# Kernel tuning notes

Measured on AMD Instinct MI355X. Metric: run time of the kernel, lower is better.

## Reference

```python
import jax, jax.numpy as jnp
import numpy as np

EPS = 1e-10

def setup_inputs() -> dict:
    key = jax.random.key(0)
    k0, k1, k2, k3, k4, k5 = jax.random.split(key, 6)
    B, S, V, C, D = 256, 20, 20000, 20, 64
    support_set_images = jax.random.uniform(k0, (B, S, V), dtype=jnp.float32)
    support_set_y_one_hot = jax.nn.one_hot(jax.random.randint(k1, (B, S), 0, C), C, dtype=jnp.float32)
    target_image = jax.random.uniform(k2, (B, V), dtype=jnp.float32)
    target_y = jax.random.randint(k3, (B,), 0, C)
    W = jax.random.normal(k4, (D, V), dtype=jnp.float32) * (1.0 / np.sqrt(V).astype(np.float32))
    b = jax.random.normal(k5, (D,), dtype=jnp.float32) * 0.01
    return dict(support_set_images=support_set_images,
                support_set_y_one_hot=support_set_y_one_hot,
                target_image=target_image, target_y=target_y, W=W, b=b)


def reference(support_set_images, support_set_y_one_hot, target_image, target_y, W, b):
    # SentenceEncoder (Linear vocab->64), applied to each support item and the target.
    sup = jnp.einsum('bsv,dv->bsd', support_set_images, W) + b        # [B,S,64]
    tgt = target_image @ W.T + b                                      # [B,64]

    # DistanceNetwork: dot(target, support) * rsqrt(clamp(||support||^2, eps))
    # (only the support vector's magnitude is normalized -- faithful to source).
    mag = jax.lax.rsqrt(jnp.clip(jnp.sum(sup * sup, axis=-1), EPS, None))  # [B,S]
    dots = jnp.einsum('bsd,bd->bs', sup, tgt)                              # [B,S]
    similarities = dots * mag                                              # [B,S]

    # AttentionalClassify: softmax over support, weighted combine of labels.
    attn = jax.nn.softmax(similarities, axis=-1)                           # [B,S]
    preds = jnp.einsum('bs,bsc->bc', attn, support_set_y_one_hot)          # [B,C]

    indices = jnp.argmax(preds, axis=1)
    accuracy = jnp.mean((indices == target_y).astype(jnp.float32))
    # F.cross_entropy applies log_softmax to preds (even though preds are already pdfs).
    logp = jax.nn.log_softmax(preds, axis=-1)
    crossentropy_loss = -jnp.mean(jnp.take_along_axis(logp, target_y[:, None], axis=1))
    return accuracy, crossentropy_loss
```

## Files before the change

### kernel.cpp

```cpp
#include <hip/hip_runtime.h>
#include <hip/hip_bf16.h>
#include <math.h>

#define B_  256
#define S_  20
#define V_  20000
#define C_  20
#define D_  64
#define MTOT (B_*S_ + B_)
#define KSPLIT 10
#define NK32 625

typedef __bf16 bf16x8 __attribute__((ext_vector_type(8)));
typedef float  f32x4  __attribute__((ext_vector_type(4)));

__device__ __forceinline__ void split8(const float4 a, const float4 b,
                                       uint4& hi, uint4& lo) {
    const float f[8] = {a.x, a.y, a.z, a.w, b.x, b.y, b.z, b.w};
    unsigned int h[8]; float r[8];
#pragma unroll
    for (int j = 0; j < 8; ++j) {
        const unsigned int u = __float_as_uint(f[j]);
        h[j] = u & 0xFFFF0000u;
        r[j] = f[j] - __uint_as_float(h[j]);
    }
    hi.x = (h[0] >> 16) | h[1];
    hi.y = (h[2] >> 16) | h[3];
    hi.z = (h[4] >> 16) | h[5];
    hi.w = (h[6] >> 16) | h[7];
    lo.x = (__float_as_uint(r[0]) >> 16) | (__float_as_uint(r[1]) & 0xFFFF0000u);
    lo.y = (__float_as_uint(r[2]) >> 16) | (__float_as_uint(r[3]) & 0xFFFF0000u);
    lo.z = (__float_as_uint(r[4]) >> 16) | (__float_as_uint(r[5]) & 0xFFFF0000u);
    lo.w = (__float_as_uint(r[6]) >> 16) | (__float_as_uint(r[7]) & 0xFFFF0000u);
}

__global__ __launch_bounds__(256)
void wconv_kernel(const float* __restrict__ W,
                  uint4* __restrict__ Wfh, uint4* __restrict__ Wfl) {
    const int g    = blockIdx.x * 256 + threadIdx.x;
    const int lane = g & 63;
    const int tt   = (g >> 6) & 3;
    const int c    = g >> 8;
    const int ln = lane & 15, qd = lane >> 4;
    const float* src = W + (size_t)(16 * tt + ln) * V_ + c * 32 + qd * 8;
    const float4 a = *(const float4*)src;
    const float4 b = *(const float4*)(src + 4);
    uint4 h, l; split8(a, b, h, l);
    Wfh[g] = h; Wfl[g] = l;
}

__device__ __forceinline__ void ldx(const float* xrow, int c, float4& r0, float4& r1) {
    const float* p = xrow + (size_t)c * 32;
    r0 = *(const float4*)p;
    r1 = *(const float4*)(p + 4);
}
__device__ __forceinline__ void ldw(const uint4* bh, const uint4* bl, int c,
                                    uint4* wh, uint4* wl) {
    const uint4* ph = bh + (size_t)c * 256;
    const uint4* pl = bl + (size_t)c * 256;
#pragma unroll
    for (int tt = 0; tt < 4; ++tt) { wh[tt] = ph[tt * 64]; wl[tt] = pl[tt * 64]; }
}
__device__ __forceinline__ void step(const float4 x0, const float4 x1,
                                     const uint4* wh, const uint4* wl, f32x4* acc) {
    uint4 hu, lu; split8(x0, x1, hu, lu);
    const bf16x8 ah = *(const bf16x8*)&hu;
    const bf16x8 al = *(const bf16x8*)&lu;
#pragma unroll
    for (int tt = 0; tt < 4; ++tt) {
        const bf16x8 bh = *(const bf16x8*)&wh[tt];
        const bf16x8 bl = *(const bf16x8*)&wl[tt];
        acc[tt] = __builtin_amdgcn_mfma_f32_16x16x32_bf16(ah, bh, acc[tt], 0, 0, 0);
        acc[tt] = __builtin_amdgcn_mfma_f32_16x16x32_bf16(ah, bl, acc[tt], 0, 0, 0);
        acc[tt] = __builtin_amdgcn_mfma_f32_16x16x32_bf16(al, bh, acc[tt], 0, 0, 0);
    }
}

__global__ __launch_bounds__(256)
void gemm2_kernel(const float* __restrict__ sup,
                  const float* __restrict__ tgtim,
                  const uint4* __restrict__ Wfh,
                  const uint4* __restrict__ Wfl,
                  float* __restrict__ Ep) {
    const int bmx = blockIdx.x;
    const int bk  = blockIdx.y;
    const int t = threadIdx.x;
    const int w = t >> 6, lane = t & 63;
    const int ln = lane & 15, qd = lane >> 4;
    const int m0 = bmx * 64;

    const float* xbase = (m0 < B_*S_)
        ? (sup   + (size_t)m0 * V_)
        : (tgtim + (size_t)(m0 - B_*S_) * V_);
    const float* xrow = xbase + (size_t)(16 * w + ln) * V_ + qd * 8;
    const uint4* wbh = Wfh + lane;
    const uint4* wbl = Wfl + lane;

    const int nk = (bk < 5) ? 63 : 62;
    const int c0 = bk * 62 + ((bk < 5) ? bk : 5);

    f32x4 acc[4];
#pragma unroll
    for (int i = 0; i < 4; ++i) acc[i] = (f32x4){0.f, 0.f, 0.f, 0.f};

    float4 xa0, xa1, xc0, xc1;
    uint4 wha[4], wla[4], whb[4], wlb[4];

    ldx(xrow, c0, xa0, xa1);
    ldw(wbh, wbl, c0, wha, wla);

    int i = 0;
    for (; i + 2 <= nk; i += 2) {
        const int c1 = c0 + i + 1;
        ldx(xrow, c1, xc0, xc1);
        ldw(wbh, wbl, c1, whb, wlb);
        step(xa0, xa1, wha, wla, acc);
        const int c2 = c0 + ((i + 2 < nk) ? (i + 2) : (i + 1));
        ldx(xrow, c2, xa0, xa1);
        ldw(wbh, wbl, c2, wha, wla);
        step(xc0, xc1, whb, wlb, acc);
    }
    if (i < nk) step(xa0, xa1, wha, wla, acc);

    float* dst = Ep + ((size_t)bk * MTOT + m0 + 16 * w + qd * 4) * D_ + ln;
#pragma unroll
    for (int tt = 0; tt < 4; ++tt)
#pragma unroll
        for (int r = 0; r < 4; ++r)
            dst[(size_t)r * D_ + 16 * tt] = acc[tt][r];
}

__global__ __launch_bounds__(256)
void reduce_kernel(float* __restrict__ Ep) {
    const size_t i = (size_t)blockIdx.x * 256 + threadIdx.x;
    const size_t stride = (size_t)MTOT * D_;
    float4 s = *(const float4*)(Ep + i * 4);
#pragma unroll
    for (int p = 1; p < KSPLIT; ++p) {
        const float4 v = *(const float4*)(Ep + p * stride + i * 4);
        s.x += v.x; s.y += v.y; s.z += v.z; s.w += v.w;
    }
    *(float4*)(Ep + i * 4) = s;
}

__global__ __launch_bounds__(64)
void phase2_kernel(const float* __restrict__ E0,
                   const float* __restrict__ bias,
                   const float* __restrict__ onehot,
                   const int*   __restrict__ ty_,
                   float* __restrict__ res) {
    const int b = blockIdx.x;
    const int d = threadIdx.x;
    const float bv = bias[d];

    float supv[S_];
#pragma unroll
    for (int s = 0; s < S_; ++s)
        supv[s] = E0[((size_t)b * S_ + s) * D_ + d] + bv;
    float tg = E0[((size_t)(B_ * S_) + b) * D_ + d] + bv;

    float sims[S_];
#pragma unroll
    for (int s = 0; s < S_; ++s) {
        float q = supv[s] * supv[s];
        float r = supv[s] * tg;
#pragma unroll
        for (int off = 32; off; off >>= 1) {
            q += __shfl_xor(q, off);
            r += __shfl_xor(r, off);
        }
        sims[s] = r * rsqrtf(fmaxf(q, 1e-10f));
    }

    float mx = sims[0];
#pragma unroll
    for (int s = 1; s < S_; ++s) mx = fmaxf(mx, sims[s]);
    float se = 0.f;
#pragma unroll
    for (int s = 0; s < S_; ++s) { sims[s] = expf(sims[s] - mx); se += sims[s]; }
    const float inv = 1.f / se;

    float pc = -INFINITY;
    if (d < C_) {
        pc = 0.f;
#pragma unroll
        for (int s = 0; s < S_; ++s)
            pc += sims[s] * inv * onehot[((size_t)b * S_ + s) * C_ + d];
    }

    float v = pc;
    int idx = (d < C_) ? d : (1 << 30);
#pragma unroll
    for (int off = 32; off; off >>= 1) {
        const float ov = __shfl_xor(v, off);
        const int   oi = __shfl_xor(idx, off);
        if (ov > v || (ov == v && oi < idx)) { v = ov; idx = oi; }
    }
    float e = (d < C_) ? expf(pc - v) : 0.f;
#pragma unroll
    for (int off = 32; off; off >>= 1) e += __shfl_xor(e, off);
    const float lse = v + logf(e);

    const int ty = ty_[b];
    const float pty = __shfl(pc, ty);

    if (d == 0) {
        res[b]      = (idx == ty) ? 1.f : 0.f;
        res[B_ + b] = lse - pty;
    }
}

__global__ __launch_bounds__(64)
void phase3_kernel(const float* __restrict__ res, float* __restrict__ out) {
    const int t = threadIdx.x;
    float c = 0.f, l = 0.f;
#pragma unroll
    for (int i = 0; i < 4; ++i) {
        c += res[t + 64 * i];
        l += res[B_ + t + 64 * i];
    }
#pragma unroll
    for (int off = 32; off; off >>= 1) {
        c += __shfl_xor(c, off);
        l += __shfl_xor(l, off);
    }
    if (t == 0) {
        out[0] = c * (1.f / 256.f);
        out[1] = l * (1.f / 256.f);
    }
}

extern "C" void kernel_launch(void* const* d_in, const int* in_sizes, int n_in,
                              void* d_out, int out_size, void* d_ws, size_t ws_size,
                              hipStream_t stream) {
    const float* sup    = (const float*)d_in[0];
    const float* onehot = (const float*)d_in[1];
    const float* tgtim  = (const float*)d_in[2];
    const int*   ty     = (const int*)  d_in[3];
    const float* W      = (const float*)d_in[4];
    const float* bias   = (const float*)d_in[5];

    float* Ep  = (float*)d_ws;
    float* res = Ep + (size_t)KSPLIT * MTOT * D_;
    uint4* Wfh = (uint4*)(res + 512);
    uint4* Wfl = Wfh + (size_t)NK32 * 4 * 64;
    float* out = (float*)d_out;

    wconv_kernel<<<625, 256, 0, stream>>>(W, Wfh, Wfl);
    gemm2_kernel<<<dim3(84, KSPLIT), 256, 0, stream>>>(sup, tgtim, Wfh, Wfl, Ep);
    reduce_kernel<<<(MTOT * D_ / 4) / 256, 256, 0, stream>>>(Ep);
    phase2_kernel<<<B_, 64, 0, stream>>>(Ep, bias, onehot, ty, res);
    phase3_kernel<<<1, 64, 0, stream>>>(res, out);
}
```

Baseline: 666.4 us.

## Give each wave four 16-row A tiles to reuse W fragments; raise K-split to 25

The GEMM kernel now has each wave compute 64 rows (four 16-row MFMA tiles) instead of 16, so each loaded W hi/lo fragment is reused across four A tiles. This cuts W traffic per FLOP. To keep enough blocks, the K-split rises from 10 to 25, giving 21x25 blocks. In exchange, register pressure goes up (16 accumulator tiles plus double-buffered A), the partial-sum buffer grows, and the reduce kernel must sum 25 partials.

```diff
diff --git a/kernel.cpp b/kernel.cpp
--- a/kernel.cpp
+++ b/kernel.cpp
@@ -8,8 +8,9 @@
 #define C_  20
 #define D_  64
 #define MTOT (B_*S_ + B_)
-#define KSPLIT 10
+#define KSPLIT 25
 #define NK32 625
+#define NKC  25
 
 typedef __bf16 bf16x8 __attribute__((ext_vector_type(8)));
 typedef float  f32x4  __attribute__((ext_vector_type(4)));
@@ -49,35 +50,8 @@
     Wfh[g] = h; Wfl[g] = l;
 }
 
-__device__ __forceinline__ void ldx(const float* xrow, int c, float4& r0, float4& r1) {
-    const float* p = xrow + (size_t)c * 32;
-    r0 = *(const float4*)p;
-    r1 = *(const float4*)(p + 4);
-}
-__device__ __forceinline__ void ldw(const uint4* bh, const uint4* bl, int c,
-                                    uint4* wh, uint4* wl) {
-    const uint4* ph = bh + (size_t)c * 256;
-    const uint4* pl = bl + (size_t)c * 256;
-#pragma unroll
-    for (int tt = 0; tt < 4; ++tt) { wh[tt] = ph[tt * 64]; wl[tt] = pl[tt * 64]; }
-}
-__device__ __forceinline__ void step(const float4 x0, const float4 x1,
-                                     const uint4* wh, const uint4* wl, f32x4* acc) {
-    uint4 hu, lu; split8(x0, x1, hu, lu);
-    const bf16x8 ah = *(const bf16x8*)&hu;
-    const bf16x8 al = *(const bf16x8*)&lu;
-#pragma unroll
-    for (int tt = 0; tt < 4; ++tt) {
-        const bf16x8 bh = *(const bf16x8*)&wh[tt];
-        const bf16x8 bl = *(const bf16x8*)&wl[tt];
-        acc[tt] = __builtin_amdgcn_mfma_f32_16x16x32_bf16(ah, bh, acc[tt], 0, 0, 0);
-        acc[tt] = __builtin_amdgcn_mfma_f32_16x16x32_bf16(ah, bl, acc[tt], 0, 0, 0);
-        acc[tt] = __builtin_amdgcn_mfma_f32_16x16x32_bf16(al, bh, acc[tt], 0, 0, 0);
-    }
-}
-
-__global__ __launch_bounds__(256)
-void gemm2_kernel(const float* __restrict__ sup,
+__global__ __launch_bounds__(256, 2)
+void gemm3_kernel(const float* __restrict__ sup,
                   const float* __restrict__ tgtim,
                   const uint4* __restrict__ Wfh,
                   const uint4* __restrict__ Wfl,
@@ -87,47 +61,88 @@
     const int t = threadIdx.x;
     const int w = t >> 6, lane = t & 63;
     const int ln = lane & 15, qd = lane >> 4;
-    const int m0 = bmx * 64;
-
-    const float* xbase = (m0 < B_*S_)
-        ? (sup   + (size_t)m0 * V_)
-        : (tgtim + (size_t)(m0 - B_*S_) * V_);
-    const float* xrow = xbase + (size_t)(16 * w + ln) * V_ + qd * 8;
+    const int mrow0 = bmx * 256 + w * 64;
+
+    const float* xbase = (mrow0 < B_*S_)
+        ? (sup   + (size_t)mrow0 * V_)
+        : (tgtim + (size_t)(mrow0 - B_*S_) * V_);
+    const float* xr0 = xbase + (size_t)ln * V_ + qd * 8;
+    const float* xr1 = xr0 + (size_t)16 * V_;
+    const float* xr2 = xr1 + (size_t)16 * V_;
+    const float* xr3 = xr2 + (size_t)16 * V_;
     const uint4* wbh = Wfh + lane;
     const uint4* wbl = Wfl + lane;
-
-    const int nk = (bk < 5) ? 63 : 62;
-    const int c0 = bk * 62 + ((bk < 5) ? bk : 5);
-
-    f32x4 acc[4];
-#pragma unroll
-    for (int i = 0; i < 4; ++i) acc[i] = (f32x4){0.f, 0.f, 0.f, 0.f};
-
-    float4 xa0, xa1, xc0, xc1;
-    uint4 wha[4], wla[4], whb[4], wlb[4];
-
-    ldx(xrow, c0, xa0, xa1);
-    ldw(wbh, wbl, c0, wha, wla);
-
-    int i = 0;
-    for (; i + 2 <= nk; i += 2) {
-        const int c1 = c0 + i + 1;
-        ldx(xrow, c1, xc0, xc1);
-        ldw(wbh, wbl, c1, whb, wlb);
-        step(xa0, xa1, wha, wla, acc);
-        const int c2 = c0 + ((i + 2 < nk) ? (i + 2) : (i + 1));
-        ldx(xrow, c2, xa0, xa1);
-        ldw(wbh, wbl, c2, wha, wla);
-        step(xc0, xc1, whb, wlb, acc);
-    }
-    if (i < nk) step(xa0, xa1, wha, wla, acc);
-
-    float* dst = Ep + ((size_t)bk * MTOT + m0 + 16 * w + qd * 4) * D_ + ln;
-#pragma unroll
-    for (int tt = 0; tt < 4; ++tt)
-#pragma unroll
-        for (int r = 0; r < 4; ++r)
-            dst[(size_t)r * D_ + 16 * tt] = acc[tt][r];
+    const int c0 = bk * NKC;
+
+    f32x4 acc[4][4];
+#pragma unroll
+    for (int i = 0; i < 4; ++i)
+#pragma unroll
+        for (int j = 0; j < 4; ++j) acc[i][j] = (f32x4){0.f, 0.f, 0.f, 0.f};
+
+    float4 aA[4][2], aB[4][2];
+    uint4 whA[4], wlA[4], whB[4], wlB[4];
+
+#define LDA(buf, c) do {                                                      \
+    const size_t off_ = (size_t)(c) * 32;                                     \
+    buf[0][0] = *(const float4*)(xr0 + off_);                                 \
+    buf[0][1] = *(const float4*)(xr0 + off_ + 4);                             \
+    buf[1][0] = *(const float4*)(xr1 + off_);                                 \
+    buf[1][1] = *(const float4*)(xr1 + off_ + 4);                             \
+    buf[2][0] = *(const float4*)(xr2 + off_);                                 \
+    buf[2][1] = *(const float4*)(xr2 + off_ + 4);                             \
+    buf[3][0] = *(const float4*)(xr3 + off_);                                 \
+    buf[3][1] = *(const float4*)(xr3 + off_ + 4);                             \
+} while (0)
+
+#define LDW(bh_, bl_, c) do {                                                 \
+    const uint4* ph_ = wbh + (size_t)(c) * 256;                               \
+    const uint4* pl_ = wbl + (size_t)(c) * 256;                               \
+    _Pragma("unroll")                                                         \
+    for (int tt = 0; tt < 4; ++tt) { bh_[tt] = ph_[tt*64]; bl_[tt] = pl_[tt*64]; } \
+} while (0)
+
+#define STEP(abuf, bh_, bl_) do {                                             \
+    _Pragma("unroll")                                                         \
+    for (int af = 0; af < 4; ++af) {                                          \
+        uint4 hu_, lu_; split8(abuf[af][0], abuf[af][1], hu_, lu_);           \
+        const bf16x8 ah_ = *(const bf16x8*)&hu_;                              \
+        const bf16x8 al_ = *(const bf16x8*)&lu_;                              \
+        _Pragma("unroll")                                                     \
+        for (int tt = 0; tt < 4; ++tt) {                                      \
+            const bf16x8 bh2_ = *(const bf16x8*)&bh_[tt];                     \
+            const bf16x8 bl2_ = *(const bf16x8*)&bl_[tt];                     \
+            acc[af][tt] = __builtin_amdgcn_mfma_f32_16x16x32_bf16(ah_, bh2_, acc[af][tt], 0, 0, 0); \
+            acc[af][tt] = __builtin_amdgcn_mfma_f32_16x16x32_bf16(ah_, bl2_, acc[af][tt], 0, 0, 0); \
+            acc[af][tt] = __builtin_amdgcn_mfma_f32_16x16x32_bf16(al_, bh2_, acc[af][tt], 0, 0, 0); \
+        }                                                                     \
+    }                                                                         \
+} while (0)
+
+    LDA(aA, c0); LDW(whA, wlA, c0);
+#pragma unroll 1
+    for (int ii = 0; ii < (NKC - 1) / 2; ++ii) {
+        const int c1 = c0 + 2 * ii + 1;
+        LDA(aB, c1); LDW(whB, wlB, c1);
+        STEP(aA, whA, wlA);
+        const int c2 = c0 + 2 * ii + 2;
+        LDA(aA, c2); LDW(whA, wlA, c2);
+        STEP(aB, whB, wlB);
+    }
+    STEP(aA, whA, wlA);
+
+#undef LDA
+#undef LDW
+#undef STEP
+
+    float* dst = Ep + ((size_t)bk * MTOT + mrow0 + qd * 4) * D_ + ln;
+#pragma unroll
+    for (int af = 0; af < 4; ++af)
+#pragma unroll
+        for (int tt = 0; tt < 4; ++tt)
+#pragma unroll
+            for (int r = 0; r < 4; ++r)
+                dst[(size_t)(af * 16 + r) * D_ + 16 * tt] = acc[af][tt][r];
 }
 
 __global__ __launch_bounds__(256)
@@ -247,7 +262,7 @@
     float* out = (float*)d_out;
 
     wconv_kernel<<<625, 256, 0, stream>>>(W, Wfh, Wfl);
-    gemm2_kernel<<<dim3(84, KSPLIT), 256, 0, stream>>>(sup, tgtim, Wfh, Wfl, Ep);
+    gemm3_kernel<<<dim3(21, KSPLIT), 256, 0, stream>>>(sup, tgtim, Wfh, Wfl, Ep);
     reduce_kernel<<<(MTOT * D_ / 4) / 256, 256, 0, stream>>>(Ep);
     phase2_kernel<<<B_, 64, 0, stream>>>(Ep, bias, onehot, ty, res);
     phase3_kernel<<<1, 64, 0, stream>>>(res, out);
```

Result: faster. 647.8 us (-2.8%).
